# Kernel optimization log

Measured on AMD Instinct MI355X. Metric: run time of the kernel, lower is better.

Reference implementation:

```python
import jax, jax.numpy as jnp
import numpy as np

N_HEADS = 16
HEAD_DIM = 128
ROPE_BASE = 50000.0
EPS = 1e-06


def _rotate_half(x):
    half = x.shape[-1] // 2
    return jnp.concatenate([-x[..., half:], x[..., :half]], axis=-1)


def _rms_norm(x, w):
    rms = jnp.sqrt(jnp.mean(x * x, axis=-1, keepdims=True) + EPS)
    return w * (x / rms)


def _rope_tables(n, dim, dtype):
    inv_freq = 1.0 / (ROPE_BASE ** (jnp.arange(0, dim, 2, dtype=jnp.float32) / dim))
    t = jnp.arange(n, dtype=jnp.float32)
    freqs = jnp.outer(t, inv_freq)          # [n, dim/2]
    emb = jnp.concatenate([freqs, freqs], axis=-1)  # [n, dim]
    return jnp.cos(emb).astype(dtype), jnp.sin(emb).astype(dtype)


def setup_inputs() -> dict:
    key = jax.random.key(0)
    ks = jax.random.split(key, 5)
    B, n, d = 2, 2048, 2048
    inner = N_HEADS * HEAD_DIM
    s = 1.0 / np.sqrt(d)
    return {
        "x": jax.random.normal(ks[0], (B, n, d), jnp.float32),
        "Wq": jax.random.normal(ks[1], (d, inner), jnp.float32) * s,
        "Wk": jax.random.normal(ks[2], (d, inner), jnp.float32) * s,
        "Wv": jax.random.normal(ks[3], (d, inner), jnp.float32) * s,
        "Wo": jax.random.normal(ks[4], (inner, d), jnp.float32) * s,
        "qn_w": jnp.ones((inner,), jnp.float32),
        "kn_w": jnp.ones((inner,), jnp.float32),
    }


def reference(x, Wq, Wk, Wv, Wo, qn_w, kn_w):
    B, n, d = x.shape
    # QKV projections (no bias)
    q = x @ Wq
    k = x @ Wk
    v = x @ Wv
    # QK RMSNorm over full inner_dim (as in the torch module)
    q = _rms_norm(q, qn_w)
    k = _rms_norm(k, kn_w)
    # [B, H, n, Dh]
    q = q.reshape(B, n, N_HEADS, HEAD_DIM).transpose(0, 2, 1, 3)
    k = k.reshape(B, n, N_HEADS, HEAD_DIM).transpose(0, 2, 1, 3)
    v = v.reshape(B, n, N_HEADS, HEAD_DIM).transpose(0, 2, 1, 3)
    # RoPE (rotary_dim == head_dim -> full rotation)
    cos, sin = _rope_tables(n, HEAD_DIM, x.dtype)  # [n, Dh]
    cos = cos[None, None]
    sin = sin[None, None]
    q = q * cos + _rotate_half(q) * sin
    k = k * cos + _rotate_half(k) * sin
    # Causal SDPA
    scale = 1.0 / np.sqrt(HEAD_DIM)
    scores = jnp.einsum("bhqd,bhkd->bhqk", q, k) * scale
    causal = jnp.tril(jnp.ones((n, n), dtype=bool))
    scores = jnp.where(causal, scores, jnp.finfo(scores.dtype).min)
    attn = jax.nn.softmax(scores, axis=-1)
    out = jnp.einsum("bhqk,bhkd->bhqd", attn, v)
    out = out.transpose(0, 2, 1, 3).reshape(B, n, N_HEADS * HEAD_DIM)
    return out @ Wo
```

## Files before the change

kernel.cpp:

```cpp
#include <hip/hip_runtime.h>

typedef unsigned short u16;
typedef unsigned int u32;
typedef __attribute__((ext_vector_type(8))) short short8;
typedef __attribute__((ext_vector_type(4))) float f32x4;
typedef __attribute__((ext_vector_type(16))) float f32x16;
typedef __attribute__((ext_vector_type(4))) u32 u32x4;

typedef __attribute__((address_space(3))) unsigned int as3u32;
typedef __attribute__((address_space(1))) unsigned int as1u32;

__device__ __forceinline__ void gld16(void* lds, const void* g) {
    __builtin_amdgcn_global_load_lds((as1u32*)(void*)g, (as3u32*)lds, 16, 0, 0);
}

__device__ inline float bf2f(u16 u) {
    u32 v = ((u32)u) << 16;
    return __builtin_bit_cast(float, v);
}
__device__ inline u16 f2bf(float f) {
    u32 u = __builtin_bit_cast(u32, f);
    u32 r = u + 0x7FFF + ((u >> 16) & 1);
    return (u16)(r >> 16);
}
__device__ __forceinline__ u32 cvtpk_bf16(float lo, float hi) {
    u32 r;
    asm("v_cvt_pk_bf16_f32 %0, %1, %2" : "=v"(r) : "v"(lo), "v"(hi));
    return r;
}
__device__ inline void unpack8(uint4 v, float* f) {
    u32 a[4] = {v.x, v.y, v.z, v.w};
#pragma unroll
    for (int i = 0; i < 4; ++i) {
        f[2 * i]     = bf2f((u16)(a[i] & 0xffff));
        f[2 * i + 1] = bf2f((u16)(a[i] >> 16));
    }
}

__global__ __launch_bounds__(256) void cast_f32_bf16(const float* __restrict__ in,
                                                     u16* __restrict__ out, int n) {
    int i = (blockIdx.x * 256 + threadIdx.x) * 8;
    if (i >= n) return;
    float4 a = *(const float4*)&in[i];
    float4 b = *(const float4*)&in[i + 4];
    u16 o[8];
    o[0] = f2bf(a.x); o[1] = f2bf(a.y); o[2] = f2bf(a.z); o[3] = f2bf(a.w);
    o[4] = f2bf(b.x); o[5] = f2bf(b.y); o[6] = f2bf(b.z); o[7] = f2bf(b.w);
    *(uint4*)&out[i] = *(uint4*)o;
}

__global__ __launch_bounds__(256) void transpose_cast4(const float* __restrict__ Wq,
                                                       const float* __restrict__ Wk,
                                                       const float* __restrict__ Wv,
                                                       const float* __restrict__ Wo,
                                                       u16* __restrict__ Wtqkv,
                                                       u16* __restrict__ Wot) {
    __shared__ float tile[64][65];
    const float* in;
    u16* out;
    switch (blockIdx.z) {
        case 0:  in = Wq; out = Wtqkv;            break;
        case 1:  in = Wk; out = Wtqkv + 4194304;  break;
        case 2:  in = Wv; out = Wtqkv + 8388608;  break;
        default: in = Wo; out = Wot;              break;
    }
    const int n0 = blockIdx.x * 64, k0 = blockIdx.y * 64;
    const int t = threadIdx.x;
    const int lr = t >> 4, lc = (t & 15) * 4;
#pragma unroll
    for (int rep = 0; rep < 4; ++rep) {
        float4 v = *(const float4*)&in[(size_t)(k0 + rep * 16 + lr) * 2048 + n0 + lc];
        tile[rep * 16 + lr][lc + 0] = v.x;
        tile[rep * 16 + lr][lc + 1] = v.y;
        tile[rep * 16 + lr][lc + 2] = v.z;
        tile[rep * 16 + lr][lc + 3] = v.w;
    }
    __syncthreads();
    const int nr = t >> 3, kc = (t & 7) * 8;
#pragma unroll
    for (int rep = 0; rep < 2; ++rep) {
        const int n = rep * 32 + nr;
        u16 o[8];
#pragma unroll
        for (int e = 0; e < 8; ++e) o[e] = f2bf(tile[kc + e][n]);
        *(uint4*)&out[(size_t)(n0 + n) * 2048 + k0 + kc] = *(uint4*)o;
    }
}

__global__ __launch_bounds__(256) void rope_tables(float* __restrict__ cosb,
                                                   float* __restrict__ sinb) {
    int idx = blockIdx.x * 256 + threadIdx.x;
    int pos = idx >> 6, i = idx & 63;
    float invf = __expf(-(float)i * (10.819778284410283f / 64.0f));
    float a = (float)pos * invf;
    cosb[idx] = cosf(a);
    sinb[idx] = sinf(a);
}

template <bool BF16OUT>
__global__ __launch_bounds__(256) void gemm_bt(const u16* __restrict__ A,
                                               const u16* __restrict__ Bt,
                                               void* __restrict__ Cv,
                                               int M, int N, int K) {
    __shared__ u16 As[2][128][64];
    __shared__ u16 Bs[2][128][64];
    const int bm = blockIdx.y, bn = blockIdx.x;
    const int tid = threadIdx.x;
    const int lane = tid & 63, w = tid >> 6;
    const int wm = (w >> 1) * 64, wn = (w & 1) * 64;
    const int lrow = lane & 15;
    const int sw = (lane & 7) << 4;
    const int srl = lane >> 3;
    const int ssw = ((lane & 7) * 16) ^ (srl << 4);
    const char* AB = (const char*)A;
    const char* BB = (const char*)Bt;
    const int NT = K >> 6;
    f32x4 acc[4][4] = {};

    const char* Ab[4];
    const char* Bb[4];
#pragma unroll
    for (int i = 0; i < 4; ++i) {
        const int rb = i * 32 + w * 8;
        Ab[i] = AB + ((size_t)(bm * 128 + rb + srl) * K) * 2 + ssw;
        Bb[i] = BB + ((size_t)(bn * 128 + rb + srl) * K) * 2 + ssw;
    }

#pragma unroll
    for (int i = 0; i < 4; ++i) {
        const int rb = i * 32 + w * 8;
        gld16(&As[0][rb][0], Ab[i]);
        gld16(&Bs[0][rb][0], Bb[i]);
    }

    for (int t = 0; t < NT; ++t) {
        const int buf = t & 1;
        __syncthreads();
        if (t + 1 < NT) {
            const size_t ko = (size_t)(t + 1) * 128;
#pragma unroll
            for (int i = 0; i < 4; ++i) {
                const int rb = i * 32 + w * 8;
                gld16(&As[buf ^ 1][rb][0], Ab[i] + ko);
                gld16(&Bs[buf ^ 1][rb][0], Bb[i] + ko);
            }
        }
        const char* AsB = (const char*)&As[buf][0][0];
        const char* BsB = (const char*)&Bs[buf][0][0];
#pragma unroll
        for (int kk = 0; kk < 2; ++kk) {
            const int cb = (kk * 64 + (lane >> 4) * 16) ^ sw;
            short8 af[4], bf_[4];
#pragma unroll
            for (int i = 0; i < 4; ++i)
                af[i] = *(const short8*)(AsB + (wm + i * 16 + lrow) * 128 + cb);
#pragma unroll
            for (int j = 0; j < 4; ++j)
                bf_[j] = *(const short8*)(BsB + (wn + j * 16 + lrow) * 128 + cb);
            __builtin_amdgcn_s_setprio(1);
#pragma unroll
            for (int i = 0; i < 4; ++i)
#pragma unroll
                for (int j = 0; j < 4; ++j)
                    acc[i][j] = __builtin_amdgcn_mfma_f32_16x16x32_bf16(af[i], bf_[j], acc[i][j], 0, 0, 0);
            __builtin_amdgcn_s_setprio(0);
        }
    }
    const int crow = (lane >> 4) * 4, ccol = lane & 15;
#pragma unroll
    for (int i = 0; i < 4; ++i)
#pragma unroll
        for (int j = 0; j < 4; ++j)
#pragma unroll
            for (int r = 0; r < 4; ++r) {
                size_t off = (size_t)(bm * 128 + wm + i * 16 + crow + r) * N +
                             (size_t)(bn * 128 + wn + j * 16 + ccol);
                if (BF16OUT) ((u16*)Cv)[off] = f2bf(acc[i][j][r]);
                else         ((float*)Cv)[off] = acc[i][j][r];
            }
}

__global__ __launch_bounds__(256) void norm_rope(const u16* __restrict__ qkv,
                                                 const float* __restrict__ qw,
                                                 const float* __restrict__ kw,
                                                 const float* __restrict__ cosb,
                                                 const float* __restrict__ sinb,
                                                 u16* __restrict__ Qout,
                                                 u16* __restrict__ Kout) {
    __shared__ float qf[2048];
    __shared__ float kf[2048];
    __shared__ float red[8];
    const int r = blockIdx.x;
    const int b = r >> 11, pos = r & 2047;
    const int t = threadIdx.x;
    const u16* row = qkv + (size_t)r * 6144;
    uint4 qv = *(const uint4*)&row[t * 8];
    uint4 kv = *(const uint4*)&row[2048 + t * 8];
    float qe[8], ke[8];
    unpack8(qv, qe);
    unpack8(kv, ke);
    float sq = 0.f, sk = 0.f;
#pragma unroll
    for (int e = 0; e < 8; ++e) {
        qf[t * 8 + e] = qe[e];
        kf[t * 8 + e] = ke[e];
        sq += qe[e] * qe[e];
        sk += ke[e] * ke[e];
    }
#pragma unroll
    for (int msk = 1; msk < 64; msk <<= 1) {
        sq += __shfl_xor(sq, msk);
        sk += __shfl_xor(sk, msk);
    }
    if ((t & 63) == 0) { red[t >> 6] = sq; red[4 + (t >> 6)] = sk; }
    __syncthreads();
    float ssq = red[0] + red[1] + red[2] + red[3];
    float ssk = red[4] + red[5] + red[6] + red[7];
    const float invq = 0.12751946f / sqrtf(ssq * (1.f / 2048.f) + 1e-6f);
    const float invk = 1.0f / sqrtf(ssk * (1.f / 2048.f) + 1e-6f);
    const float* ct = cosb + pos * 64;
    const float* st = sinb + pos * 64;
    u16 qo[8], ko[8];
#pragma unroll
    for (int e = 0; e < 8; ++e) {
        int c = t * 8 + e;
        int jl = c & 127;
        int hb = c & ~127;
        int jj = jl & 63;
        float cs = ct[jj], sn = st[jj];
        int pair = hb + ((jl < 64) ? jl + 64 : jl - 64);
        float sgn = (jl < 64) ? -1.f : 1.f;
        float xq = qf[c] * qw[c], pq = qf[pair] * qw[pair];
        float xk = kf[c] * kw[c], pk = kf[pair] * kw[pair];
        qo[e] = f2bf((xq * cs + sgn * pq * sn) * invq);
        ko[e] = f2bf((xk * cs + sgn * pk * sn) * invk);
    }
    const int h = (t * 8) >> 7;
    const int j0 = (t * 8) & 127;
    size_t o = ((size_t)(b * 16 + h) * 2048 + pos) * 128 + j0;
    *(uint4*)&Qout[o] = *(uint4*)qo;
    *(uint4*)&Kout[o] = *(uint4*)ko;
}

__global__ __launch_bounds__(256) void v_transpose(const u16* __restrict__ qkv,
                                                   u16* __restrict__ Vt) {
    __shared__ u16 tile[64][136];
    const int bx = blockIdx.x;
    const int pt = bx & 31, bh = bx >> 5;
    const int b = bh >> 4, h = bh & 15;
    const int pos0 = pt * 64;
    const int t = threadIdx.x;
    const int p = t >> 4, jc = (t & 15) * 8;
#pragma unroll
    for (int rep = 0; rep < 4; ++rep)
        *(uint4*)&tile[rep * 16 + p][jc] =
            *(const uint4*)&qkv[(size_t)(b * 2048 + pos0 + rep * 16 + p) * 6144 + 4096 + h * 128 + jc];
    __syncthreads();
    const int j = t >> 3, pc = (t & 7) * 8;
#pragma unroll
    for (int rep = 0; rep < 4; ++rep) {
        const int jj = rep * 32 + j;
        u16 tmp[8];
#pragma unroll
        for (int e = 0; e < 8; ++e) tmp[e] = tile[pc + e][jj];
        *(uint4*)&Vt[((size_t)bh * 128 + jj) * 2048 + pos0 + pc] = *(uint4*)tmp;
    }
}

__global__ __launch_bounds__(256, 2) void attn_fwd(const u16* __restrict__ Qr,
                                                   const u16* __restrict__ Kr,
                                                   const u16* __restrict__ Vt,
                                                   u16* __restrict__ O) {
    __shared__ u16 Ks[2][64][128];
    __shared__ u16 VsT[2][128][64];
    const int bx = blockIdx.x;
    const int g = bx >> 3;
    const int bh = (bx & 7) + 8 * (g & 3);
    const int qt = (g < 32) ? (15 - (g >> 2)) : ((g >> 2) - 8);
    const int tid = threadIdx.x;
    const int lane = tid & 63, w = tid >> 6;
    const int ql = lane & 31, h = lane >> 5;
    const char* KhB = (const char*)(Kr + (size_t)bh * 2048 * 128);
    const char* VhB = (const char*)(Vt + (size_t)bh * 128 * 2048);
    const u16* Qh = Qr + (size_t)bh * 2048 * 128;
    const int b = bh >> 4, hh = bh & 15;
    const int krl = lane >> 4;
    const int ksc = (lane & 15) * 16;
    const int vrl = lane >> 3;
    const int vsc = (lane & 7) * 16;
    const int swz = (ql & 7) << 4;

    const int q0w = qt * 128 + w * 32;
    const int qg = q0w + ql;
    short8 qb[8];
#pragma unroll
    for (int s = 0; s < 8; ++s)
        qb[s] = *(const short8*)&Qh[(size_t)qg * 128 + s * 16 + h * 8];

    f32x16 ot[4] = {};
    float m = -3e38f, ls = 0.f;
    const int kend = qt * 128 + 128;

#pragma unroll
    for (int j = 0; j < 4; ++j) {
        const int krb = w * 16 + j * 4;
        const int kr = krb + krl;
        gld16(&Ks[0][krb][0], KhB + (size_t)kr * 256 + (ksc ^ ((kr & 7) << 4)));
        const int vrb = w * 32 + j * 8;
        const int vr = vrb + vrl;
        gld16(&VsT[0][vrb][0], VhB + (size_t)vr * 4096 + (vsc ^ ((vr & 7) << 4)));
    }

    for (int k0 = 0; k0 < kend; k0 += 64) {
        const int buf = (k0 >> 6) & 1;
        __syncthreads();
        if (k0 + 64 < kend) {
            const int kn = k0 + 64;
#pragma unroll
            for (int j = 0; j < 4; ++j) {
                const int krb = w * 16 + j * 4;
                const int kr = krb + krl;
                gld16(&Ks[buf ^ 1][krb][0],
                      KhB + (size_t)(kn + kr) * 256 + (ksc ^ ((kr & 7) << 4)));
                const int vrb = w * 32 + j * 8;
                const int vr = vrb + vrl;
                gld16(&VsT[buf ^ 1][vrb][0],
                      VhB + (size_t)vr * 4096 + (size_t)kn * 2 + (vsc ^ ((vr & 7) << 4)));
            }
        }
        const char* KsB = (const char*)&Ks[buf][0][0];
        const char* VsB = (const char*)&VsT[buf][0][0];

        f32x16 st[2] = {};
#pragma unroll
        for (int s = 0; s < 8; ++s) {
            short8 kf0 = *(const short8*)(KsB + (size_t)ql * 256 + ((s * 32 + 16 * h) ^ swz));
            short8 kf1 = *(const short8*)(KsB + (size_t)(32 + ql) * 256 + ((s * 32 + 16 * h) ^ swz));
            st[0] = __builtin_amdgcn_mfma_f32_32x32x16_bf16(kf0, qb[s], st[0], 0, 0, 0);
            st[1] = __builtin_amdgcn_mfma_f32_32x32x16_bf16(kf1, qb[s], st[1], 0, 0, 0);
        }

        if (k0 + 64 > q0w) {
#pragma unroll
            for (int T = 0; T < 2; ++T)
#pragma unroll
                for (int reg = 0; reg < 16; ++reg) {
                    int c = k0 + 32 * T + (reg & 3) + 8 * (reg >> 2) + 4 * h;
                    if (c > qg) st[T][reg] = -1e30f;
                }
        }

        float mx = st[0][0];
#pragma unroll
        for (int T = 0; T < 2; ++T)
#pragma unroll
            for (int reg = 0; reg < 16; ++reg) mx = fmaxf(mx, st[T][reg]);
        mx = fmaxf(mx, __shfl_xor(mx, 32));

        if (__any(mx > m + 8.f)) {
            float mn = fmaxf(m, mx);
            float corr = exp2f(m - mn);
            m = mn;
            ls *= corr;
#pragma unroll
            for (int td = 0; td < 4; ++td)
#pragma unroll
                for (int reg = 0; reg < 16; ++reg) ot[td][reg] *= corr;
        }

        float ps = 0.f;
#pragma unroll
        for (int T = 0; T < 2; ++T)
#pragma unroll
            for (int reg = 0; reg < 16; ++reg) {
                float p = exp2f(st[T][reg] - m);
                st[T][reg] = p;
                ps += p;
            }
        ps += __shfl_xor(ps, 32);
        ls += ps;

#pragma unroll
        for (int T = 0; T < 2; ++T) {
            u32 c[4][2];
#pragma unroll
            for (int mm = 0; mm < 4; ++mm) {
                c[mm][0] = cvtpk_bf16(st[T][4 * mm + 0], st[T][4 * mm + 1]);
                c[mm][1] = cvtpk_bf16(st[T][4 * mm + 2], st[T][4 * mm + 3]);
            }
#pragma unroll
            for (int i = 0; i < 2; ++i) {
                const int ks = 2 * T + i;
                u32 a0 = c[2 * i][0], b0 = c[2 * i + 1][0];
                u32 a1 = c[2 * i][1], b1 = c[2 * i + 1][1];
                asm volatile("v_permlane32_swap_b32 %0, %1" : "+v"(a0), "+v"(b0));
                asm volatile("v_permlane32_swap_b32 %0, %1" : "+v"(a1), "+v"(b1));
                u32x4 pw = {a0, a1, b0, b1};
                short8 pf = __builtin_bit_cast(short8, pw);
#pragma unroll
                for (int td = 0; td < 4; ++td) {
                    short8 vf = *(const short8*)(VsB + (size_t)(32 * td + ql) * 128 +
                                                 ((32 * ks + 16 * h) ^ swz));
                    ot[td] = __builtin_amdgcn_mfma_f32_32x32x16_bf16(vf, pf, ot[td], 0, 0, 0);
                }
            }
        }
    }

    const float inv = 1.0f / ls;
    const size_t base = ((size_t)b * 2048 + qg) * 2048 + (size_t)hh * 128;
#pragma unroll
    for (int td = 0; td < 4; ++td)
#pragma unroll
        for (int g2 = 0; g2 < 4; ++g2) {
            ushort4 o4;
            o4.x = f2bf(ot[td][4 * g2 + 0] * inv);
            o4.y = f2bf(ot[td][4 * g2 + 1] * inv);
            o4.z = f2bf(ot[td][4 * g2 + 2] * inv);
            o4.w = f2bf(ot[td][4 * g2 + 3] * inv);
            *(ushort4*)&O[base + 32 * td + 8 * g2 + 4 * h] = o4;
        }
}

extern "C" void kernel_launch(void* const* d_in, const int* in_sizes, int n_in,
                              void* d_out, int out_size, void* d_ws, size_t ws_size,
                              hipStream_t stream) {
    const float* x   = (const float*)d_in[0];
    const float* Wq  = (const float*)d_in[1];
    const float* Wk  = (const float*)d_in[2];
    const float* Wv  = (const float*)d_in[3];
    const float* Wo  = (const float*)d_in[4];
    const float* qnw = (const float*)d_in[5];
    const float* knw = (const float*)d_in[6];

    const size_t MB = 1ull << 20;
    char* ws = (char*)d_ws;
    u16* Xbf    = (u16*)(ws + 0);
    u16* Qr     = (u16*)(ws + 0);
    u16* Wtqkv  = (u16*)(ws + 16 * MB);
    u16* Wot    = (u16*)(ws + 40 * MB);
    u16* QKV    = (u16*)(ws + 48 * MB);
    u16* AOut   = (u16*)(ws + 48 * MB);
    float* cosb = (float*)(ws + 96 * MB);
    float* sinb = (float*)(ws + 96 * MB + 524288);
    u16* Kr     = (u16*)(ws + 97 * MB);
    u16* Vt     = (u16*)(ws + 113 * MB);

    cast_f32_bf16<<<4096, 256, 0, stream>>>(x, Xbf, 4096 * 2048);
    transpose_cast4<<<dim3(32, 32, 4), 256, 0, stream>>>(Wq, Wk, Wv, Wo, Wtqkv, Wot);
    rope_tables<<<512, 256, 0, stream>>>(cosb, sinb);

    gemm_bt<true><<<dim3(48, 32), 256, 0, stream>>>(Xbf, Wtqkv, (void*)QKV, 4096, 6144, 2048);

    norm_rope<<<4096, 256, 0, stream>>>(QKV, qnw, knw, cosb, sinb, Qr, Kr);
    v_transpose<<<1024, 256, 0, stream>>>(QKV, Vt);

    attn_fwd<<<512, 256, 0, stream>>>(Qr, Kr, Vt, AOut);

    gemm_bt<false><<<dim3(16, 32), 256, 0, stream>>>(AOut, Wot, d_out, 4096, 2048, 2048);
}
```

Measured before the change: 269.4 us.

## Add 256x256-tile 512-thread GEMM for QKV projection with XCD-aware block remap

Replaces the 128x128 QKV projection GEMM with a new kernel that uses 256x256 output tiles, 8 waves per block, double-buffered direct-to-LDS loads interleaved with MFMA sub-steps, and s_setprio around the math. Block IDs are remapped so consecutive tiles land on the same XCD, which is meant to improve L2 reuse. The larger tile raises arithmetic intensity and cuts redundant global loads. In exchange it uses 128KB of LDS per block, so only one block fits per CU, and the epilogue writes scalar bf16 values rather than vectorised stores.

```diff
diff --git a/kernel.cpp b/kernel.cpp
--- a/kernel.cpp
+++ b/kernel.cpp
@@ -95,6 +95,113 @@
     float a = (float)pos * invf;
     cosb[idx] = cosf(a);
     sinb[idx] = sinf(a);
+}
+
+__global__ __launch_bounds__(512, 1) void gemm256(const u16* __restrict__ A,
+                                                  const u16* __restrict__ Bt,
+                                                  u16* __restrict__ C,
+                                                  int M, int N, int K) {
+    __shared__ u16 As[2][256][64];
+    __shared__ u16 Bs[2][256][64];
+    const int NT = K >> 6;
+    const int cpx = gridDim.x >> 3;
+    const int bid = blockIdx.x;
+    const int wg = (bid & 7) * cpx + (bid >> 3);
+    const int gm = M >> 8;
+    const int bn = wg / gm, bm = wg % gm;
+    const int tid = threadIdx.x;
+    const int lane = tid & 63, w = tid >> 6;
+    const int wr = w >> 2, wc = w & 3;
+    const int lrow = lane & 15;
+    const int sw = (lane & 7) << 4;
+    const int srl = lane >> 3;
+    const int ssw = ((lane & 7) * 16) ^ (srl << 4);
+    const size_t Kb = (size_t)K * 2;
+    const char* Asrc = (const char*)A  + (size_t)(bm * 256 + w * 16 + srl) * Kb + ssw;
+    const char* Bsrc = (const char*)Bt + (size_t)(bn * 256 + w * 16 + srl) * Kb + ssw;
+
+    f32x4 acc[8][4] = {};
+
+#pragma unroll
+    for (int H = 0; H < 2; ++H)
+#pragma unroll
+        for (int c = 0; c < 2; ++c) {
+            gld16(&As[0][H * 128 + w * 16 + c * 8][0], Asrc + (size_t)(H * 128 + c * 8) * Kb);
+            gld16(&Bs[0][H * 128 + w * 16 + c * 8][0], Bsrc + (size_t)(H * 128 + c * 8) * Kb);
+        }
+    asm volatile("s_waitcnt vmcnt(0)" ::: "memory");
+    asm volatile("s_barrier" ::: "memory");
+
+    for (int t = 0; t < NT; ++t) {
+        const int buf = t & 1;
+        const char* AsB = (const char*)&As[buf][0][0];
+        const char* BsB = (const char*)&Bs[buf][0][0];
+        const bool more = (t + 1 < NT);
+        const size_t ko = (size_t)(t + 1) * 128;
+        short8 bfr[4][2];
+#pragma unroll
+        for (int q = 0; q < 4; ++q) {
+            short8 afr[2][2];
+#pragma unroll
+            for (int e = 0; e < 2; ++e)
+#pragma unroll
+                for (int kh = 0; kh < 2; ++kh)
+                    afr[e][kh] = *(const short8*)(AsB +
+                        (wr * 128 + (2 * q + e) * 16 + lrow) * 128 +
+                        ((kh * 64 + (lane >> 4) * 16) ^ sw));
+            if (q == 0) {
+#pragma unroll
+                for (int fc = 0; fc < 4; ++fc)
+#pragma unroll
+                    for (int kh = 0; kh < 2; ++kh)
+                        bfr[fc][kh] = *(const short8*)(BsB +
+                            (wc * 64 + fc * 16 + lrow) * 128 +
+                            ((kh * 64 + (lane >> 4) * 16) ^ sw));
+            }
+            if (q == 0 && more) {
+#pragma unroll
+                for (int H = 0; H < 2; ++H)
+#pragma unroll
+                    for (int c = 0; c < 2; ++c)
+                        gld16(&As[buf ^ 1][H * 128 + w * 16 + c * 8][0],
+                              Asrc + (size_t)(H * 128 + c * 8) * Kb + ko);
+            }
+            if (q == 1 && more) {
+#pragma unroll
+                for (int H = 0; H < 2; ++H)
+#pragma unroll
+                    for (int c = 0; c < 2; ++c)
+                        gld16(&Bs[buf ^ 1][H * 128 + w * 16 + c * 8][0],
+                              Bsrc + (size_t)(H * 128 + c * 8) * Kb + ko);
+            }
+            asm volatile("s_barrier" ::: "memory");
+            __builtin_amdgcn_s_setprio(1);
+#pragma unroll
+            for (int e = 0; e < 2; ++e)
+#pragma unroll
+                for (int fc = 0; fc < 4; ++fc)
+#pragma unroll
+                    for (int kh = 0; kh < 2; ++kh)
+                        acc[2 * q + e][fc] = __builtin_amdgcn_mfma_f32_16x16x32_bf16(
+                            afr[e][kh], bfr[fc][kh], acc[2 * q + e][fc], 0, 0, 0);
+            __builtin_amdgcn_s_setprio(0);
+            if (q == 3)
+                asm volatile("s_waitcnt vmcnt(0)" ::: "memory");
+            asm volatile("s_barrier" ::: "memory");
+        }
+    }
+
+    const int crow = (lane >> 4) * 4, ccol = lane & 15;
+#pragma unroll
+    for (int fm = 0; fm < 8; ++fm)
+#pragma unroll
+        for (int fn = 0; fn < 4; ++fn)
+#pragma unroll
+            for (int r = 0; r < 4; ++r) {
+                size_t off = (size_t)(bm * 256 + wr * 128 + fm * 16 + crow + r) * N +
+                             (size_t)(bn * 256 + wc * 64 + fn * 16 + ccol);
+                C[off] = f2bf(acc[fm][fn][r]);
+            }
 }
 
 template <bool BF16OUT>
@@ -450,7 +557,7 @@
     transpose_cast4<<<dim3(32, 32, 4), 256, 0, stream>>>(Wq, Wk, Wv, Wo, Wtqkv, Wot);
     rope_tables<<<512, 256, 0, stream>>>(cosb, sinb);
 
-    gemm_bt<true><<<dim3(48, 32), 256, 0, stream>>>(Xbf, Wtqkv, (void*)QKV, 4096, 6144, 2048);
+    gemm256<<<384, 512, 0, stream>>>(Xbf, Wtqkv, QKV, 4096, 6144, 2048);
 
     norm_rope<<<4096, 256, 0, stream>>>(QKV, qnw, knw, cosb, sinb, Qr, Kr);
     v_transpose<<<1024, 256, 0, stream>>>(QKV, Vt);
```

Measured after the change: 289.3 us. +7.4%, slower.
